# Optimization experiments

Measured on AMD Instinct MI355X. Metric: run time of the kernel, lower is better.

The kernel has to match this reference:

```python
import jax, jax.numpy as jnp
import numpy as np

B, S = 512, 512
VOCAB, E, H1, H2, NTAGS = 50000, 20, 30, 50, 45


def _xavier_scale(fan_in, fan_out):
    return float(np.sqrt(2.0 / (fan_in + fan_out)))


def setup_inputs() -> dict:
    key = jax.random.key(0)
    ks = jax.random.split(key, 32)
    n = lambda i, shape, s=1.0: jax.random.normal(ks[i], shape, dtype=jnp.float32) * s
    w = 0.1  # weight scale
    emb_f1 = n(0, (VOCAB, E), w).at[0].set(0.0)  # padding_idx=0
    emb_b1 = n(1, (VOCAB, E), w).at[0].set(0.0)
    xs1 = _xavier_scale(B, H1)
    xs2 = _xavier_scale(B, H2)
    inp = {
        "x": jax.random.randint(ks[2], (B, S), 0, VOCAB, dtype=jnp.int64),
        "emb_f1": emb_f1, "emb_b1": emb_b1,
        "h0_f1": n(3, (B, H1), xs1), "c0_f1": n(4, (B, H1), xs1),
        "Wih_f1": n(5, (4 * H1, E), w), "Whh_f1": n(6, (4 * H1, H1), w),
        "bih_f1": n(7, (4 * H1,), w), "bhh_f1": n(8, (4 * H1,), w),
        "h0_b1": n(9, (B, H1), xs1), "c0_b1": n(10, (B, H1), xs1),
        "Wih_b1": n(11, (4 * H1, E), w), "Whh_b1": n(12, (4 * H1, H1), w),
        "bih_b1": n(13, (4 * H1,), w), "bhh_b1": n(14, (4 * H1,), w),
        "h0_f2": n(15, (B, H2), xs2), "c0_f2": n(16, (B, H2), xs2),
        "Wih_f2": n(17, (4 * H2, 2 * H1), w), "Whh_f2": n(18, (4 * H2, H2), w),
        "bih_f2": n(19, (4 * H2,), w), "bhh_f2": n(20, (4 * H2,), w),
        "h0_b2": n(21, (B, H2), xs2), "c0_b2": n(22, (B, H2), xs2),
        "Wih_b2": n(23, (4 * H2, 2 * H1), w), "Whh_b2": n(24, (4 * H2, H2), w),
        "bih_b2": n(25, (4 * H2,), w), "bhh_b2": n(26, (4 * H2,), w),
        "lin_w": n(27, (NTAGS, 2 * H2), w), "lin_b": n(28, (NTAGS,), w),
    }
    return inp


def _run_lstm(seq, h0, c0, Wih, Whh, bih, bhh, forward):
    """PyTorch LSTMCell recurrence over seq (B,S,D). Replicates the original's
    quirks: backward dir appends hidden states in reversed time order, and the
    (S,B,H) stack is .view()-ed into (B,S,H) without transposing."""
    b, s, _ = seq.shape
    h = h0.shape[-1]
    xs = jnp.swapaxes(seq, 0, 1)  # (S,B,D)

    def step(carry, xt):
        hh, cc = carry
        g = xt @ Wih.T + bih + hh @ Whh.T + bhh  # (B, 4H), gate order i,f,g,o
        i, f, gg, o = jnp.split(g, 4, axis=-1)
        cc = jax.nn.sigmoid(f) * cc + jax.nn.sigmoid(i) * jnp.tanh(gg)
        hh = jax.nn.sigmoid(o) * jnp.tanh(cc)
        return (hh, cc), hh

    _, hs = jax.lax.scan(step, (h0, c0), xs, reverse=not forward)  # hs[i] ~ time i
    if not forward:
        hs = hs[::-1]  # torch appended in processing (reversed-time) order
    return hs.reshape(b, s, h)  # faithful buggy view (S,B,H) -> (B,S,H)


def reference(x, emb_f1, emb_b1,
              h0_f1, c0_f1, Wih_f1, Whh_f1, bih_f1, bhh_f1,
              h0_b1, c0_b1, Wih_b1, Whh_b1, bih_b1, bhh_b1,
              h0_f2, c0_f2, Wih_f2, Whh_f2, bih_f2, bhh_f2,
              h0_b2, c0_b2, Wih_b2, Whh_b2, bih_b2, bhh_b2,
              lin_w, lin_b):
    f1 = _run_lstm(emb_f1[x], h0_f1, c0_f1, Wih_f1, Whh_f1, bih_f1, bhh_f1, True)
    b1 = _run_lstm(emb_b1[x], h0_b1, c0_b1, Wih_b1, Whh_b1, bih_b1, bhh_b1, False)
    l1 = jnp.concatenate([f1, b1], axis=2)  # (B,S,2*H1)
    f2 = _run_lstm(l1, h0_f2, c0_f2, Wih_f2, Whh_f2, bih_f2, bhh_f2, True)
    b2 = _run_lstm(l1, h0_b2, c0_b2, Wih_b2, Whh_b2, bih_b2, bhh_b2, False)
    l2 = jnp.concatenate([f2, b2], axis=2)  # (B,S,2*H2)
    return l2 @ lin_w.T + lin_b  # (B,S,NTAGS)
```

## Files before the change

### kernel.cpp

```cpp
#include <hip/hip_runtime.h>
#include <hip/hip_bf16.h>

typedef __hip_bfloat16 bf16;
typedef __attribute__((ext_vector_type(8))) short short8;
typedef __attribute__((ext_vector_type(4))) float float4v;
typedef unsigned short ushort_t;

#define BB 512
#define SS 512
#define EE 20
#define H1C 30
#define H2C 50
#define NTC 45

#define BAR() asm volatile("s_waitcnt lgkmcnt(0)\n\ts_barrier" ::: "memory")

#if __has_builtin(__builtin_amdgcn_exp2f)
#define EXP2(x) __builtin_amdgcn_exp2f(x)
#else
#define EXP2(x) exp2f(x)
#endif
#if __has_builtin(__builtin_amdgcn_rcpf)
#define RCPF(x) __builtin_amdgcn_rcpf(x)
#else
#define RCPF(x) (1.0f / (x))
#endif

__device__ __forceinline__ float sigf(float v) {
    return RCPF(1.0f + EXP2(-1.4426950408889634f * v));
}
__device__ __forceinline__ float tanh_(float v) {
    return 2.0f * RCPF(1.0f + EXP2(-2.8853900817779268f * v)) - 1.0f;
}

__device__ __forceinline__ ushort_t f2bf(float f) {
    unsigned u = __float_as_uint(f);
    unsigned r = u + 0x7FFFu + ((u >> 16) & 1u);
    return (ushort_t)(r >> 16);
}
__device__ __forceinline__ float bf2f(ushort_t s) { return __uint_as_float(((unsigned)s) << 16); }

__device__ __forceinline__ float ldG(const void* p, int i, int f32) {
    if (f32) return ((const float*)p)[i];
    return bf2f(((const ushort_t*)p)[i]);
}
__device__ __forceinline__ int ldTok(const void* x, int i, int x64) {
    const int* xi = (const int*)x;
    return x64 ? xi[2 * i] : xi[i];
}

__global__ void detect_kernel(const void* bih, const void* x, int* flags) {
    if (threadIdx.x == 0 && blockIdx.x == 0) {
        const ushort_t* u = (const ushort_t*)bih;
        int isf = 0;
        for (int i = 0; i < 120; i++) {
            float v = fabsf(bf2f(u[i]));
            if (!(v < 16.0f)) isf = 1;
        }
        flags[0] = isf;
        const int* xi = (const int*)x;
        int orv = 0;
        for (int i = 1; i < 32; i += 2) orv |= xi[i];
        flags[1] = (orv == 0) ? 1 : 0;
    }
}

struct XV4 { float v[4]; };

__global__ __launch_bounds__(128, 1) void lstm1_kernel(
    const void* __restrict__ x,
    const void* __restrict__ emb_f, const void* __restrict__ emb_b,
    const void* __restrict__ h0_f, const void* __restrict__ c0_f,
    const void* __restrict__ Wih_f, const void* __restrict__ Whh_f,
    const void* __restrict__ bih_f, const void* __restrict__ bhh_f,
    const void* __restrict__ h0_b, const void* __restrict__ c0_b,
    const void* __restrict__ Wih_b, const void* __restrict__ Whh_b,
    const void* __restrict__ bih_b, const void* __restrict__ bhh_b,
    ushort_t* __restrict__ hsf, ushort_t* __restrict__ hsb,
    const int* __restrict__ flags)
{
    const int f32v = flags[0], x64 = flags[1];
    const int wg = blockIdx.x, dir = wg >> 5, j0 = (wg & 31) << 4, tid = threadIdx.x;
    const int wave = tid >> 6, lane = tid & 63, li = lane & 15, quad = lane >> 4;

    const void* emb = dir ? emb_b : emb_f;
    const void* h0  = dir ? h0_b  : h0_f;
    const void* c0  = dir ? c0_b  : c0_f;
    const void* Wih = dir ? Wih_b : Wih_f;
    const void* Whh = dir ? Whh_b : Whh_f;
    const void* bih = dir ? bih_b : bih_f;
    const void* bhh = dir ? bhh_b : bhh_f;
    ushort_t* hs = dir ? hsb : hsf;

    __shared__ __align__(16) ushort_t Af[2][2][64][8];
    __shared__ int toks[16][SS];

    for (int idx = tid; idx < 16 * SS; idx += 128) {
        int r = idx >> 9, t = idx & (SS - 1);
        toks[r][t] = ldTok(x, (j0 + r) * SS + t, x64);
    }
    for (int idx = tid; idx < 2 * 2 * 64 * 8; idx += 128) ((ushort_t*)Af)[idx] = 0;

    const int n = wave * 16 + li;
    const bool nok = n < H1C;

    short8 bhi[4][2], blo[4][2];
    float bias_g[4];
    #pragma unroll
    for (int g = 0; g < 4; g++) {
        const int wrow = g * H1C + n;
        bias_g[g] = nok ? (ldG(bih, wrow, f32v) + ldG(bhh, wrow, f32v)) : 0.f;
        #pragma unroll
        for (int kt = 0; kt < 2; kt++) {
            short8 hi, lo;
            #pragma unroll
            for (int j = 0; j < 8; j++) {
                int k = kt * 32 + quad * 8 + j;
                float w = 0.f;
                if (nok) {
                    if (k < EE) w = ldG(Wih, wrow * EE + k, f32v);
                    else if (k < EE + H1C) w = ldG(Whh, wrow * H1C + (k - EE), f32v);
                }
                ushort_t h = f2bf(w);
                hi[j] = (short)h;
                lo[j] = (short)f2bf(w - bf2f(h));
            }
            bhi[g][kt] = hi; blo[g][kt] = lo;
        }
    }

    const int kh = EE + n;
    const int khk = kh >> 5, khg = (kh & 31) >> 3, khj = kh & 7;
    const int lrow = tid / 5, lc = tid - lrow * 5, k0 = lc * 4;
    const bool ldr = tid < 80;
    const int t0 = dir ? SS - 1 : 0, dt = dir ? -1 : 1;

    __syncthreads();

    float creg[4];
    #pragma unroll
    for (int r = 0; r < 4; r++) {
        const int m = quad * 4 + r;
        creg[r] = nok ? ldG(c0, (j0 + m) * H1C + n, f32v) : 0.f;
        ushort_t hb = nok ? f2bf(ldG(h0, (j0 + m) * H1C + n, f32v)) : 0;
        Af[0][khk][khg * 16 + m][khj] = hb;
    }
    XV4 xA, xB;
    if (ldr) {
        int tok = toks[lrow][t0];
        #pragma unroll
        for (int jj = 0; jj < 4; jj++)
            Af[0][0][(k0 >> 3) * 16 + lrow][(k0 & 7) + jj] = f2bf(ldG(emb, tok * EE + k0 + jj, f32v));
        int tok1 = toks[lrow][t0 + dt];
        #pragma unroll
        for (int jj = 0; jj < 4; jj++) xA.v[jj] = ldG(emb, tok1 * EE + k0 + jj, f32v);
    }
    __syncthreads();

    auto step = [&](int it, XV4& xin, XV4& xout) {
        const int t = t0 + dt * it;
        const int cur = it & 1, nxt = cur ^ 1;
        BAR();
        short8 af0 = *(const short8*)&Af[cur][0][lane][0];
        short8 af1 = *(const short8*)&Af[cur][1][lane][0];
        if (ldr && it + 2 < SS) {
            int tok = toks[lrow][t + 2 * dt];
            #pragma unroll
            for (int jj = 0; jj < 4; jj++) xout.v[jj] = ldG(emb, tok * EE + k0 + jj, f32v);
        }
        float4v acc[4];
        #pragma unroll
        for (int g = 0; g < 4; g++) {
            float4v a; a[0] = a[1] = a[2] = a[3] = bias_g[g];
            a = __builtin_amdgcn_mfma_f32_16x16x32_bf16(af0, bhi[g][0], a, 0, 0, 0);
            a = __builtin_amdgcn_mfma_f32_16x16x32_bf16(af0, blo[g][0], a, 0, 0, 0);
            a = __builtin_amdgcn_mfma_f32_16x16x32_bf16(af1, bhi[g][1], a, 0, 0, 0);
            a = __builtin_amdgcn_mfma_f32_16x16x32_bf16(af1, blo[g][1], a, 0, 0, 0);
            acc[g] = a;
        }
        ushort_t hb[4];
        #pragma unroll
        for (int r = 0; r < 4; r++) {
            float gi = acc[0][r], gf = acc[1][r], gg = acc[2][r], go = acc[3][r];
            float c = sigf(gf) * creg[r] + sigf(gi) * tanh_(gg);
            float h = sigf(go) * tanh_(c);
            creg[r] = c;
            hb[r] = nok ? f2bf(h) : 0;
            hs[((size_t)(j0 + quad * 4 + r) * SS + t) * 32 + n] = hb[r];
        }
        if (it + 1 < SS) {
            #pragma unroll
            for (int r = 0; r < 4; r++) Af[nxt][khk][khg * 16 + quad * 4 + r][khj] = hb[r];
            if (ldr) {
                #pragma unroll
                for (int jj = 0; jj < 4; jj++)
                    Af[nxt][0][(k0 >> 3) * 16 + lrow][(k0 & 7) + jj] = f2bf(xin.v[jj]);
            }
        }
    };
    for (int it = 0; it < SS; it += 2) { step(it, xA, xB); step(it + 1, xB, xA); }
}

__global__ __launch_bounds__(256, 1) void lstm2_kernel(
    const ushort_t* __restrict__ hs1f, const ushort_t* __restrict__ hs1b,
    const void* __restrict__ h0_f, const void* __restrict__ c0_f,
    const void* __restrict__ Wih_f, const void* __restrict__ Whh_f,
    const void* __restrict__ bih_f, const void* __restrict__ bhh_f,
    const void* __restrict__ h0_b, const void* __restrict__ c0_b,
    const void* __restrict__ Wih_b, const void* __restrict__ Whh_b,
    const void* __restrict__ bih_b, const void* __restrict__ bhh_b,
    ushort_t* __restrict__ hsf, ushort_t* __restrict__ hsb,
    const int* __restrict__ flags)
{
    const int f32v = flags[0];
    const int wg = blockIdx.x, dir = wg >> 5, cb = (wg & 31) << 4, tid = threadIdx.x;
    const int wave = tid >> 6, lane = tid & 63, li = lane & 15, quad = lane >> 4;

    const void* h0  = dir ? h0_b  : h0_f;
    const void* c0  = dir ? c0_b  : c0_f;
    const void* Wih = dir ? Wih_b : Wih_f;
    const void* Whh = dir ? Whh_b : Whh_f;
    const void* bih = dir ? bih_b : bih_f;
    const void* bhh = dir ? bhh_b : bhh_f;
    ushort_t* hs = dir ? hsb : hsf;

    __shared__ __align__(16) ushort_t Af[2][4][64][8];
    for (int idx = tid; idx < 2 * 4 * 64 * 8; idx += 256) ((ushort_t*)Af)[idx] = 0;

    const int n = wave * 16 + li;
    const bool nok = n < H2C;

    short8 bhi[4][4], blo[4][4];
    float bias_g[4];
    #pragma unroll
    for (int g = 0; g < 4; g++) {
        const int wrow = g * H2C + n;
        bias_g[g] = nok ? (ldG(bih, wrow, f32v) + ldG(bhh, wrow, f32v)) : 0.f;
        #pragma unroll
        for (int kt = 0; kt < 4; kt++) {
            short8 hi, lo;
            #pragma unroll
            for (int j = 0; j < 8; j++) {
                int k = kt * 32 + quad * 8 + j;
                float w = 0.f;
                if (nok) {
                    if (k < H1C) w = ldG(Wih, wrow * (2 * H1C) + k, f32v);
                    else if (k >= 32 && k < 32 + H1C) w = ldG(Wih, wrow * (2 * H1C) + H1C + (k - 32), f32v);
                    else if (k >= 64 && k < 64 + H2C) w = ldG(Whh, wrow * H2C + (k - 64), f32v);
                }
                ushort_t h = f2bf(w);
                hi[j] = (short)h;
                lo[j] = (short)f2bf(w - bf2f(h));
            }
            bhi[g][kt] = hi; blo[g][kt] = lo;
        }
    }

    const int kh = 64 + n;
    const int khk = kh >> 5, khg = (kh & 31) >> 3, khj = kh & 7;
    const int lrow = tid >> 4, k0 = (tid & 15) * 4;
    const int t0 = dir ? SS - 1 : 0, dt = dir ? -1 : 1;

    auto loadX = [&](int c) -> ushort4 {
        const int a = cb + lrow;
        if (k0 < 32)
            return *(const ushort4*)&hs1f[((size_t)c * SS + a) * 32 + k0];
        else
            return *(const ushort4*)&hs1b[((size_t)c * SS + (SS - 1 - a)) * 32 + (k0 - 32)];
    };

    __syncthreads();

    float creg[4];
    #pragma unroll
    for (int r = 0; r < 4; r++) {
        const int m = quad * 4 + r;
        creg[r] = nok ? ldG(c0, (cb + m) * H2C + n, f32v) : 0.f;
        ushort_t hb = nok ? f2bf(ldG(h0, (cb + m) * H2C + n, f32v)) : 0;
        Af[0][khk][khg * 16 + m][khj] = hb;
    }
    {
        ushort4 xi = loadX(t0);
        const int kg = (k0 & 31) >> 3, kt = k0 >> 5, jb = k0 & 7;
        Af[0][kt][kg * 16 + lrow][jb + 0] = xi.x;
        Af[0][kt][kg * 16 + lrow][jb + 1] = xi.y;
        Af[0][kt][kg * 16 + lrow][jb + 2] = xi.z;
        Af[0][kt][kg * 16 + lrow][jb + 3] = xi.w;
    }
    ushort4 xA = loadX(t0 + dt), xB;
    __syncthreads();

    auto step = [&](int it, ushort4& xin, ushort4& xout) {
        const int c = t0 + dt * it;
        const int cur = it & 1, nxt = cur ^ 1;
        BAR();
        short8 af[4];
        #pragma unroll
        for (int kt = 0; kt < 4; kt++) af[kt] = *(const short8*)&Af[cur][kt][lane][0];
        if (it + 2 < SS) xout = loadX(c + 2 * dt);
        float4v acc[4];
        #pragma unroll
        for (int g = 0; g < 4; g++) {
            float4v a; a[0] = a[1] = a[2] = a[3] = bias_g[g];
            #pragma unroll
            for (int kt = 0; kt < 4; kt++) {
                a = __builtin_amdgcn_mfma_f32_16x16x32_bf16(af[kt], bhi[g][kt], a, 0, 0, 0);
                a = __builtin_amdgcn_mfma_f32_16x16x32_bf16(af[kt], blo[g][kt], a, 0, 0, 0);
            }
            acc[g] = a;
        }
        ushort_t hb[4];
        #pragma unroll
        for (int r = 0; r < 4; r++) {
            float gi = acc[0][r], gf = acc[1][r], gg = acc[2][r], go = acc[3][r];
            float cc = sigf(gf) * creg[r] + sigf(gi) * tanh_(gg);
            float h = sigf(go) * tanh_(cc);
            creg[r] = cc;
            hb[r] = nok ? f2bf(h) : 0;
        }
        ushort4 h4; h4.x = hb[0]; h4.y = hb[1]; h4.z = hb[2]; h4.w = hb[3];
        *(ushort4*)&hs[((size_t)c * 64 + n) * SS + cb + quad * 4] = h4;
        if (it + 1 < SS) {
            #pragma unroll
            for (int r = 0; r < 4; r++) Af[nxt][khk][khg * 16 + quad * 4 + r][khj] = hb[r];
            const int kg = (k0 & 31) >> 3, kt = k0 >> 5, jb = k0 & 7;
            Af[nxt][kt][kg * 16 + lrow][jb + 0] = xin.x;
            Af[nxt][kt][kg * 16 + lrow][jb + 1] = xin.y;
            Af[nxt][kt][kg * 16 + lrow][jb + 2] = xin.z;
            Af[nxt][kt][kg * 16 + lrow][jb + 3] = xin.w;
        }
    };
    for (int it = 0; it < SS; it += 2) { step(it, xA, xB); step(it + 1, xB, xA); }
}

__global__ __launch_bounds__(256) void lin_kernel(
    const ushort_t* __restrict__ hs2f, const ushort_t* __restrict__ hs2b,
    const void* __restrict__ lw, const void* __restrict__ lb,
    void* __restrict__ out, const int* __restrict__ flags)
{
    const int f32v = flags[0];
    const int tid = threadIdx.x, wave = tid >> 6, lane = tid & 63, li = lane & 15, quad = lane >> 4;

    __shared__ __align__(16) ushort_t Af[4][4][64][8];
    for (int idx = tid; idx < 4 * 4 * 64 * 8; idx += 256) ((ushort_t*)Af)[idx] = 0;

    short8 bhi[3][4], blo[3][4];
    float biasv[3];
    #pragma unroll
    for (int nt = 0; nt < 3; nt++) {
        const int nn = nt * 16 + li;
        const bool nok = nn < NTC;
        biasv[nt] = nok ? ldG(lb, nn, f32v) : 0.f;
        #pragma unroll
        for (int kt = 0; kt < 4; kt++) {
            short8 hi, lo;
            #pragma unroll
            for (int j = 0; j < 8; j++) {
                int k = kt * 32 + quad * 8 + j;
                float w = 0.f;
                if (nok) {
                    if (k < H2C) w = ldG(lw, nn * 100 + k, f32v);
                    else if (k >= 64 && k < 64 + H2C) w = ldG(lw, nn * 100 + 50 + (k - 64), f32v);
                }
                ushort_t h = f2bf(w);
                hi[j] = (short)h;
                lo[j] = (short)f2bf(w - bf2f(h));
            }
            bhi[nt][kt] = hi; blo[nt][kt] = lo;
        }
    }

    const int P0 = blockIdx.x * 64;
    const int i = P0 >> 9, j0 = P0 & 511;
    __syncthreads();
    for (int idx = tid; idx < 100 * 32; idx += 256) {
        const int kk = idx >> 5, pj = (idx & 31) * 2;
        unsigned v;
        int k;
        if (kk < H2C) {
            v = *(const unsigned*)&hs2f[((size_t)i * 64 + kk) * SS + j0 + pj];
            k = kk;
        } else {
            v = *(const unsigned*)&hs2b[((size_t)(SS - 1 - i) * 64 + (kk - H2C)) * SS + j0 + pj];
            k = 64 + (kk - H2C);
        }
        const int kt = k >> 5, kg = (k & 31) >> 3, j = k & 7;
        Af[pj >> 4][kt][kg * 16 + (pj & 15)][j] = (ushort_t)(v & 0xFFFF);
        Af[pj >> 4][kt][kg * 16 + ((pj + 1) & 15)][j] = (ushort_t)(v >> 16);
    }
    __syncthreads();

    short8 af[4];
    #pragma unroll
    for (int kt = 0; kt < 4; kt++) af[kt] = *(const short8*)&Af[wave][kt][lane][0];
    #pragma unroll
    for (int nt = 0; nt < 3; nt++) {
        float4v a; a[0] = a[1] = a[2] = a[3] = biasv[nt];
        #pragma unroll
        for (int kt = 0; kt < 4; kt++) {
            a = __builtin_amdgcn_mfma_f32_16x16x32_bf16(af[kt], bhi[nt][kt], a, 0, 0, 0);
            a = __builtin_amdgcn_mfma_f32_16x16x32_bf16(af[kt], blo[nt][kt], a, 0, 0, 0);
        }
        const int nn = nt * 16 + li;
        if (nn < NTC) {
            #pragma unroll
            for (int reg = 0; reg < 4; reg++) {
                const int prow = wave * 16 + quad * 4 + reg;
                const size_t op = (size_t)(P0 + prow) * NTC + nn;
                if (f32v) ((float*)out)[op] = a[reg];
                else      ((ushort_t*)out)[op] = f2bf(a[reg]);
            }
        }
    }
}

extern "C" void kernel_launch(void* const* d_in, const int* in_sizes, int n_in,
                              void* d_out, int out_size, void* d_ws, size_t ws_size,
                              hipStream_t stream)
{
    const void* x      = d_in[0];
    const void* emb_f1 = d_in[1];
    const void* emb_b1 = d_in[2];
    const void* h0_f1  = d_in[3];
    const void* c0_f1  = d_in[4];
    const void* Wih_f1 = d_in[5];
    const void* Whh_f1 = d_in[6];
    const void* bih_f1 = d_in[7];
    const void* bhh_f1 = d_in[8];
    const void* h0_b1  = d_in[9];
    const void* c0_b1  = d_in[10];
    const void* Wih_b1 = d_in[11];
    const void* Whh_b1 = d_in[12];
    const void* bih_b1 = d_in[13];
    const void* bhh_b1 = d_in[14];
    const void* h0_f2  = d_in[15];
    const void* c0_f2  = d_in[16];
    const void* Wih_f2 = d_in[17];
    const void* Whh_f2 = d_in[18];
    const void* bih_f2 = d_in[19];
    const void* bhh_f2 = d_in[20];
    const void* h0_b2  = d_in[21];
    const void* c0_b2  = d_in[22];
    const void* Wih_b2 = d_in[23];
    const void* Whh_b2 = d_in[24];
    const void* bih_b2 = d_in[25];
    const void* bhh_b2 = d_in[26];
    const void* lin_w  = d_in[27];
    const void* lin_b  = d_in[28];

    int* flags = (int*)d_ws;
    ushort_t* hs1f = (ushort_t*)((char*)d_ws + 256);
    ushort_t* hs1b = hs1f + (size_t)BB * SS * 32;
    ushort_t* hs2f = hs1b + (size_t)BB * SS * 32;
    ushort_t* hs2b = hs2f + (size_t)SS * 64 * BB;

    detect_kernel<<<1, 64, 0, stream>>>(bih_f1, x, flags);
    lstm1_kernel<<<64, 128, 0, stream>>>(x, emb_f1, emb_b1,
        h0_f1, c0_f1, Wih_f1, Whh_f1, bih_f1, bhh_f1,
        h0_b1, c0_b1, Wih_b1, Whh_b1, bih_b1, bhh_b1, hs1f, hs1b, flags);
    lstm2_kernel<<<64, 256, 0, stream>>>(hs1f, hs1b,
        h0_f2, c0_f2, Wih_f2, Whh_f2, bih_f2, bhh_f2,
        h0_b2, c0_b2, Wih_b2, Whh_b2, bih_b2, bhh_b2, hs2f, hs2b, flags);
    lin_kernel<<<(BB * SS) / 64, 256, 0, stream>>>(hs2f, hs2b, lin_w, lin_b, d_out, flags);
}
```

Measured before the change: 1.003 ms.

## Process two 16-row batch groups per workgroup in both LSTM kernels

```diff
diff --git a/kernel.cpp b/kernel.cpp
--- a/kernel.cpp
+++ b/kernel.cpp
@@ -80,7 +80,7 @@
     const int* __restrict__ flags)
 {
     const int f32v = flags[0], x64 = flags[1];
-    const int wg = blockIdx.x, dir = wg >> 5, j0 = (wg & 31) << 4, tid = threadIdx.x;
+    const int wg = blockIdx.x, dir = wg >> 4, j0 = (wg & 15) << 5, tid = threadIdx.x;
     const int wave = tid >> 6, lane = tid & 63, li = lane & 15, quad = lane >> 4;
 
     const void* emb = dir ? emb_b : emb_f;
@@ -92,14 +92,14 @@
     const void* bhh = dir ? bhh_b : bhh_f;
     ushort_t* hs = dir ? hsb : hsf;
 
-    __shared__ __align__(16) ushort_t Af[2][2][64][8];
-    __shared__ int toks[16][SS];
-
-    for (int idx = tid; idx < 16 * SS; idx += 128) {
+    __shared__ __align__(16) ushort_t Af[2][2][2][64][8];
+    __shared__ int toks[32][SS];
+
+    for (int idx = tid; idx < 32 * SS; idx += 128) {
         int r = idx >> 9, t = idx & (SS - 1);
         toks[r][t] = ldTok(x, (j0 + r) * SS + t, x64);
     }
-    for (int idx = tid; idx < 2 * 2 * 64 * 8; idx += 128) ((ushort_t*)Af)[idx] = 0;
+    for (int idx = tid; idx < 2 * 2 * 2 * 64 * 8; idx += 128) ((ushort_t*)Af)[idx] = 0;
 
     const int n = wave * 16 + li;
     const bool nok = n < H1C;
@@ -133,68 +133,95 @@
     const int khk = kh >> 5, khg = (kh & 31) >> 3, khj = kh & 7;
     const int lrow = tid / 5, lc = tid - lrow * 5, k0 = lc * 4;
     const bool ldr = tid < 80;
+    const int lkt = k0 >> 5, lkg = (k0 & 31) >> 3, ljb = k0 & 7;
     const int t0 = dir ? SS - 1 : 0, dt = dir ? -1 : 1;
 
     __syncthreads();
 
-    float creg[4];
-    #pragma unroll
-    for (int r = 0; r < 4; r++) {
-        const int m = quad * 4 + r;
-        creg[r] = nok ? ldG(c0, (j0 + m) * H1C + n, f32v) : 0.f;
-        ushort_t hb = nok ? f2bf(ldG(h0, (j0 + m) * H1C + n, f32v)) : 0;
-        Af[0][khk][khg * 16 + m][khj] = hb;
-    }
-    XV4 xA, xB;
+    float creg[2][4];
+    #pragma unroll
+    for (int grp = 0; grp < 2; grp++) {
+        #pragma unroll
+        for (int r = 0; r < 4; r++) {
+            const int m = quad * 4 + r, row = j0 + grp * 16 + m;
+            creg[grp][r] = nok ? ldG(c0, row * H1C + n, f32v) : 0.f;
+            ushort_t hb = nok ? f2bf(ldG(h0, row * H1C + n, f32v)) : 0;
+            Af[0][grp][khk][khg * 16 + m][khj] = hb;
+        }
+    }
+    XV4 xA[2], xB[2];
     if (ldr) {
-        int tok = toks[lrow][t0];
-        #pragma unroll
-        for (int jj = 0; jj < 4; jj++)
-            Af[0][0][(k0 >> 3) * 16 + lrow][(k0 & 7) + jj] = f2bf(ldG(emb, tok * EE + k0 + jj, f32v));
-        int tok1 = toks[lrow][t0 + dt];
-        #pragma unroll
-        for (int jj = 0; jj < 4; jj++) xA.v[jj] = ldG(emb, tok1 * EE + k0 + jj, f32v);
+        #pragma unroll
+        for (int grp = 0; grp < 2; grp++) {
+            int tok = toks[grp * 16 + lrow][t0];
+            ushort4 v;
+            v.x = f2bf(ldG(emb, tok * EE + k0 + 0, f32v));
+            v.y = f2bf(ldG(emb, tok * EE + k0 + 1, f32v));
+            v.z = f2bf(ldG(emb, tok * EE + k0 + 2, f32v));
+            v.w = f2bf(ldG(emb, tok * EE + k0 + 3, f32v));
+            *(ushort4*)&Af[0][grp][lkt][lkg * 16 + lrow][ljb] = v;
+            int tok1 = toks[grp * 16 + lrow][t0 + dt];
+            #pragma unroll
+            for (int jj = 0; jj < 4; jj++) xA[grp].v[jj] = ldG(emb, tok1 * EE + k0 + jj, f32v);
+        }
     }
     __syncthreads();
 
-    auto step = [&](int it, XV4& xin, XV4& xout) {
+    auto step = [&](int it, XV4* xin, XV4* xout) {
         const int t = t0 + dt * it;
         const int cur = it & 1, nxt = cur ^ 1;
         BAR();
-        short8 af0 = *(const short8*)&Af[cur][0][lane][0];
-        short8 af1 = *(const short8*)&Af[cur][1][lane][0];
+        short8 af[2][2];
+        #pragma unroll
+        for (int grp = 0; grp < 2; grp++) {
+            af[grp][0] = *(const short8*)&Af[cur][grp][0][lane][0];
+            af[grp][1] = *(const short8*)&Af[cur][grp][1][lane][0];
+        }
         if (ldr && it + 2 < SS) {
-            int tok = toks[lrow][t + 2 * dt];
-            #pragma unroll
-            for (int jj = 0; jj < 4; jj++) xout.v[jj] = ldG(emb, tok * EE + k0 + jj, f32v);
-        }
-        float4v acc[4];
-        #pragma unroll
-        for (int g = 0; g < 4; g++) {
-            float4v a; a[0] = a[1] = a[2] = a[3] = bias_g[g];
-            a = __builtin_amdgcn_mfma_f32_16x16x32_bf16(af0, bhi[g][0], a, 0, 0, 0);
-            a = __builtin_amdgcn_mfma_f32_16x16x32_bf16(af0, blo[g][0], a, 0, 0, 0);
-            a = __builtin_amdgcn_mfma_f32_16x16x32_bf16(af1, bhi[g][1], a, 0, 0, 0);
-            a = __builtin_amdgcn_mfma_f32_16x16x32_bf16(af1, blo[g][1], a, 0, 0, 0);
-            acc[g] = a;
-        }
-        ushort_t hb[4];
-        #pragma unroll
-        for (int r = 0; r < 4; r++) {
-            float gi = acc[0][r], gf = acc[1][r], gg = acc[2][r], go = acc[3][r];
-            float c = sigf(gf) * creg[r] + sigf(gi) * tanh_(gg);
-            float h = sigf(go) * tanh_(c);
-            creg[r] = c;
-            hb[r] = nok ? f2bf(h) : 0;
-            hs[((size_t)(j0 + quad * 4 + r) * SS + t) * 32 + n] = hb[r];
-        }
-        if (it + 1 < SS) {
-            #pragma unroll
-            for (int r = 0; r < 4; r++) Af[nxt][khk][khg * 16 + quad * 4 + r][khj] = hb[r];
-            if (ldr) {
+            #pragma unroll
+            for (int grp = 0; grp < 2; grp++) {
+                int tok = toks[grp * 16 + lrow][t + 2 * dt];
                 #pragma unroll
-                for (int jj = 0; jj < 4; jj++)
-                    Af[nxt][0][(k0 >> 3) * 16 + lrow][(k0 & 7) + jj] = f2bf(xin.v[jj]);
+                for (int jj = 0; jj < 4; jj++) xout[grp].v[jj] = ldG(emb, tok * EE + k0 + jj, f32v);
+            }
+        }
+        float4v acc[2][4];
+        #pragma unroll
+        for (int grp = 0; grp < 2; grp++) {
+            #pragma unroll
+            for (int g = 0; g < 4; g++) {
+                float4v a; a[0] = a[1] = a[2] = a[3] = bias_g[g];
+                a = __builtin_amdgcn_mfma_f32_16x16x32_bf16(af[grp][0], bhi[g][0], a, 0, 0, 0);
+                a = __builtin_amdgcn_mfma_f32_16x16x32_bf16(af[grp][0], blo[g][0], a, 0, 0, 0);
+                a = __builtin_amdgcn_mfma_f32_16x16x32_bf16(af[grp][1], bhi[g][1], a, 0, 0, 0);
+                a = __builtin_amdgcn_mfma_f32_16x16x32_bf16(af[grp][1], blo[g][1], a, 0, 0, 0);
+                acc[grp][g] = a;
+            }
+        }
+        #pragma unroll
+        for (int grp = 0; grp < 2; grp++) {
+            ushort_t hb[4];
+            #pragma unroll
+            for (int r = 0; r < 4; r++) {
+                float gi = acc[grp][0][r], gf = acc[grp][1][r], gg = acc[grp][2][r], go = acc[grp][3][r];
+                float c = sigf(gf) * creg[grp][r] + sigf(gi) * tanh_(gg);
+                float h = sigf(go) * tanh_(c);
+                creg[grp][r] = c;
+                hb[r] = nok ? f2bf(h) : 0;
+                hs[((size_t)(j0 + grp * 16 + quad * 4 + r) * SS + t) * 32 + n] = hb[r];
+            }
+            if (it + 1 < SS) {
+                #pragma unroll
+                for (int r = 0; r < 4; r++) Af[nxt][grp][khk][khg * 16 + quad * 4 + r][khj] = hb[r];
+            }
+        }
+        if (ldr && it + 1 < SS) {
+            #pragma unroll
+            for (int grp = 0; grp < 2; grp++) {
+                ushort4 v;
+                v.x = f2bf(xin[grp].v[0]); v.y = f2bf(xin[grp].v[1]);
+                v.z = f2bf(xin[grp].v[2]); v.w = f2bf(xin[grp].v[3]);
+                *(ushort4*)&Af[nxt][grp][lkt][lkg * 16 + lrow][ljb] = v;
             }
         }
     };
@@ -213,7 +240,7 @@
     const int* __restrict__ flags)
 {
     const int f32v = flags[0];
-    const int wg = blockIdx.x, dir = wg >> 5, cb = (wg & 31) << 4, tid = threadIdx.x;
+    const int wg = blockIdx.x, dir = wg >> 4, cb = (wg & 15) << 5, tid = threadIdx.x;
     const int wave = tid >> 6, lane = tid & 63, li = lane & 15, quad = lane >> 4;
 
     const void* h0  = dir ? h0_b  : h0_f;
@@ -224,8 +251,8 @@
     const void* bhh = dir ? bhh_b : bhh_f;
     ushort_t* hs = dir ? hsb : hsf;
 
-    __shared__ __align__(16) ushort_t Af[2][4][64][8];
-    for (int idx = tid; idx < 2 * 4 * 64 * 8; idx += 256) ((ushort_t*)Af)[idx] = 0;
+    __shared__ __align__(16) ushort_t Af[2][2][4][64][8];
+    for (int idx = tid; idx < 2 * 2 * 4 * 64 * 8; idx += 256) ((ushort_t*)Af)[idx] = 0;
 
     const int n = wave * 16 + li;
     const bool nok = n < H2C;
@@ -259,10 +286,11 @@
     const int kh = 64 + n;
     const int khk = kh >> 5, khg = (kh & 31) >> 3, khj = kh & 7;
     const int lrow = tid >> 4, k0 = (tid & 15) * 4;
+    const int lkt = k0 >> 5, lkg = (k0 & 31) >> 3, ljb = k0 & 7;
     const int t0 = dir ? SS - 1 : 0, dt = dir ? -1 : 1;
 
-    auto loadX = [&](int c) -> ushort4 {
-        const int a = cb + lrow;
+    auto loadX = [&](int c, int grp) -> ushort4 {
+        const int a = cb + grp * 16 + lrow;
         if (k0 < 32)
             return *(const ushort4*)&hs1f[((size_t)c * SS + a) * 32 + k0];
         else
@@ -271,63 +299,71 @@
 
     __syncthreads();
 
-    float creg[4];
-    #pragma unroll
-    for (int r = 0; r < 4; r++) {
-        const int m = quad * 4 + r;
-        creg[r] = nok ? ldG(c0, (cb + m) * H2C + n, f32v) : 0.f;
-        ushort_t hb = nok ? f2bf(ldG(h0, (cb + m) * H2C + n, f32v)) : 0;
-        Af[0][khk][khg * 16 + m][khj] = hb;
-    }
-    {
-        ushort4 xi = loadX(t0);
-        const int kg = (k0 & 31) >> 3, kt = k0 >> 5, jb = k0 & 7;
-        Af[0][kt][kg * 16 + lrow][jb + 0] = xi.x;
-        Af[0][kt][kg * 16 + lrow][jb + 1] = xi.y;
-        Af[0][kt][kg * 16 + lrow][jb + 2] = xi.z;
-        Af[0][kt][kg * 16 + lrow][jb + 3] = xi.w;
-    }
-    ushort4 xA = loadX(t0 + dt), xB;
+    float creg[2][4];
+    #pragma unroll
+    for (int grp = 0; grp < 2; grp++) {
+        #pragma unroll
+        for (int r = 0; r < 4; r++) {
+            const int m = quad * 4 + r, row = cb + grp * 16 + m;
+            creg[grp][r] = nok ? ldG(c0, row * H2C + n, f32v) : 0.f;
+            ushort_t hb = nok ? f2bf(ldG(h0, row * H2C + n, f32v)) : 0;
+            Af[0][grp][khk][khg * 16 + m][khj] = hb;
+        }
+    }
+    #pragma unroll
+    for (int grp = 0; grp < 2; grp++) {
+        ushort4 xi = loadX(t0, grp);
+        *(ushort4*)&Af[0][grp][lkt][lkg * 16 + lrow][ljb] = xi;
+    }
+    ushort4 xA[2], xB[2];
+    xA[0] = loadX(t0 + dt, 0); xA[1] = loadX(t0 + dt, 1);
     __syncthreads();
 
-    auto step = [&](int it, ushort4& xin, ushort4& xout) {
+    auto step = [&](int it, ushort4* xin, ushort4* xout) {
         const int c = t0 + dt * it;
         const int cur = it & 1, nxt = cur ^ 1;
         BAR();
-        short8 af[4];
-        #pragma unroll
-        for (int kt = 0; kt < 4; kt++) af[kt] = *(const short8*)&Af[cur][kt][lane][0];
-        if (it + 2 < SS) xout = loadX(c + 2 * dt);
-        float4v acc[4];
-        #pragma unroll
-        for (int g = 0; g < 4; g++) {
-            float4v a; a[0] = a[1] = a[2] = a[3] = bias_g[g];
-            #pragma unroll
-            for (int kt = 0; kt < 4; kt++) {
-                a = __builtin_amdgcn_mfma_f32_16x16x32_bf16(af[kt], bhi[g][kt], a, 0, 0, 0);
-                a = __builtin_amdgcn_mfma_f32_16x16x32_bf16(af[kt], blo[g][kt], a, 0, 0, 0);
-            }
-            acc[g] = a;
-        }
-        ushort_t hb[4];
-        #pragma unroll
-        for (int r = 0; r < 4; r++) {
-            float gi = acc[0][r], gf = acc[1][r], gg = acc[2][r], go = acc[3][r];
-            float cc = sigf(gf) * creg[r] + sigf(gi) * tanh_(gg);
-            float h = sigf(go) * tanh_(cc);
-            creg[r] = cc;
-            hb[r] = nok ? f2bf(h) : 0;
-        }
-        ushort4 h4; h4.x = hb[0]; h4.y = hb[1]; h4.z = hb[2]; h4.w = hb[3];
-        *(ushort4*)&hs[((size_t)c * 64 + n) * SS + cb + quad * 4] = h4;
-        if (it + 1 < SS) {
-            #pragma unroll
-            for (int r = 0; r < 4; r++) Af[nxt][khk][khg * 16 + quad * 4 + r][khj] = hb[r];
-            const int kg = (k0 & 31) >> 3, kt = k0 >> 5, jb = k0 & 7;
-            Af[nxt][kt][kg * 16 + lrow][jb + 0] = xin.x;
-            Af[nxt][kt][kg * 16 + lrow][jb + 1] = xin.y;
-            Af[nxt][kt][kg * 16 + lrow][jb + 2] = xin.z;
-            Af[nxt][kt][kg * 16 + lrow][jb + 3] = xin.w;
+        short8 af[2][4];
+        #pragma unroll
+        for (int grp = 0; grp < 2; grp++)
+            #pragma unroll
+            for (int kt = 0; kt < 4; kt++) af[grp][kt] = *(const short8*)&Af[cur][grp][kt][lane][0];
+        if (it + 2 < SS) {
+            xout[0] = loadX(c + 2 * dt, 0);
+            xout[1] = loadX(c + 2 * dt, 1);
+        }
+        float4v acc[2][4];
+        #pragma unroll
+        for (int grp = 0; grp < 2; grp++) {
+            #pragma unroll
+            for (int g = 0; g < 4; g++) {
+                float4v a; a[0] = a[1] = a[2] = a[3] = bias_g[g];
+                #pragma unroll
+                for (int kt = 0; kt < 4; kt++) {
+                    a = __builtin_amdgcn_mfma_f32_16x16x32_bf16(af[grp][kt], bhi[g][kt], a, 0, 0, 0);
+                    a = __builtin_amdgcn_mfma_f32_16x16x32_bf16(af[grp][kt], blo[g][kt], a, 0, 0, 0);
+                }
+                acc[grp][g] = a;
+            }
+        }
+        #pragma unroll
+        for (int grp = 0; grp < 2; grp++) {
+            ushort_t hb[4];
+            #pragma unroll
+            for (int r = 0; r < 4; r++) {
+                float gi = acc[grp][0][r], gf = acc[grp][1][r], gg = acc[grp][2][r], go = acc[grp][3][r];
+                float cc = sigf(gf) * creg[grp][r] + sigf(gi) * tanh_(gg);
+                float h = sigf(go) * tanh_(cc);
+                creg[grp][r] = cc;
+                hb[r] = nok ? f2bf(h) : 0;
+            }
+            ushort4 h4; h4.x = hb[0]; h4.y = hb[1]; h4.z = hb[2]; h4.w = hb[3];
+            *(ushort4*)&hs[((size_t)c * 64 + n) * SS + cb + grp * 16 + quad * 4] = h4;
+            if (it + 1 < SS) {
+                #pragma unroll
+                for (int r = 0; r < 4; r++) Af[nxt][grp][khk][khg * 16 + quad * 4 + r][khj] = hb[r];
+                *(ushort4*)&Af[nxt][grp][lkt][lkg * 16 + lrow][ljb] = xin[grp];
+            }
         }
     };
     for (int it = 0; it < SS; it += 2) { step(it, xA, xB); step(it + 1, xB, xA); }
@@ -455,10 +491,10 @@
     ushort_t* hs2b = hs2f + (size_t)SS * 64 * BB;
 
     detect_kernel<<<1, 64, 0, stream>>>(bih_f1, x, flags);
-    lstm1_kernel<<<64, 128, 0, stream>>>(x, emb_f1, emb_b1,
+    lstm1_kernel<<<32, 128, 0, stream>>>(x, emb_f1, emb_b1,
         h0_f1, c0_f1, Wih_f1, Whh_f1, bih_f1, bhh_f1,
         h0_b1, c0_b1, Wih_b1, Whh_b1, bih_b1, bhh_b1, hs1f, hs1b, flags);
-    lstm2_kernel<<<64, 256, 0, stream>>>(hs1f, hs1b,
+    lstm2_kernel<<<32, 256, 0, stream>>>(hs1f, hs1b,
         h0_f2, c0_f2, Wih_f2, Whh_f2, bih_f2, bhh_f2,
         h0_b2, c0_b2, Wih_b2, Whh_b2, bih_b2, bhh_b2, hs2f, hs2b, flags);
     lin_kernel<<<(BB * SS) / 64, 256, 0, stream>>>(hs2f, hs2b, lin_w, lin_b, d_out, flags);
```

Result: slower. 1.734 ms (+72.9%).
